# Kernel optimization log

Hardware: AMD Instinct MI355X
Metric: run time of the kernel (lower is better)

## Reference

```python
import jax, jax.numpy as jnp
import numpy as np

NUM_TOKENS = 8192
CODEBOOK_DIM = 64
ENC_CH = 512
DEC_CH = 512
B, H, W = 16, 32, 32


def setup_inputs() -> dict:
    key = jax.random.key(0)
    ks = jax.random.split(key, 6)
    return {
        "x": jax.random.normal(ks[0], (B, ENC_CH, H, W), dtype=jnp.float32),
        "w_in": jax.random.normal(ks[1], (CODEBOOK_DIM, ENC_CH), dtype=jnp.float32) * 0.05,
        "b_in": jax.random.normal(ks[2], (CODEBOOK_DIM,), dtype=jnp.float32) * 0.05,
        "embedding": jax.random.normal(ks[3], (NUM_TOKENS, CODEBOOK_DIM), dtype=jnp.float32),
        "w_out": jax.random.normal(ks[4], (DEC_CH, CODEBOOK_DIM), dtype=jnp.float32) * 0.05,
        "b_out": jax.random.normal(ks[5], (DEC_CH,), dtype=jnp.float32) * 0.05,
    }


def reference(x, w_in, b_in, embedding, w_out, b_out):
    # encoder projection: 1x1 conv == channel matmul. x: [B,C,H,W] -> [B,d,H,W]
    z = jnp.einsum('bchw,dc->bdhw', x, w_in) + b_in[None, :, None, None]

    # VectorQuantizer.forward -----------------------------------------
    # permute to channels-last and flatten: [B,H,W,d] -> [N,d]
    inputs = jnp.transpose(z, (0, 2, 3, 1))  # [B,H,W,d]
    flat = inputs.reshape(-1, CODEBOOK_DIM)  # [N,d]

    # squared L2 distances to every codebook entry: [N,K]
    distances = (jnp.sum(flat ** 2, axis=1, keepdims=True)
                 + jnp.sum(embedding ** 2, axis=1)[None, :]
                 - 2.0 * flat @ embedding.T)
    indices = jnp.argmin(distances, axis=1)  # [N] int

    # one-hot @ embedding in the original == direct gather
    quantized = jnp.take(embedding, indices, axis=0).reshape(inputs.shape)

    # straight-through estimator
    quantized = inputs + jax.lax.stop_gradient(quantized - inputs)
    tokens = jnp.transpose(quantized, (0, 3, 1, 2))  # [B,d,H,W]

    # decoder projection: 1x1 conv
    projected = jnp.einsum('bdhw,od->bohw', tokens, w_out) + b_out[None, :, None, None]
    return projected, indices
```

## Files before the change

kernel.cpp:

```cpp
#include <hip/hip_runtime.h>

#define NROWS 16384
#define DDIM 64
#define KCB 8192
#define CIN 512
#define OUTC 512
#define OUT_MAIN 8388608

typedef float f4 __attribute__((ext_vector_type(4)));
typedef float f32x16 __attribute__((ext_vector_type(16)));
typedef __bf16 bf16x4 __attribute__((ext_vector_type(4)));
typedef __bf16 bf16x8 __attribute__((ext_vector_type(8)));

#define OFF_ZBF 0
#define OFF_EBF 1572864
#define OFF_E2H 2359296
#define OFF_PMV 2367488
#define OFF_PMI 2629632
#define ZS_STRIDE 1048576
#define ES_STRIDE 524288

__global__ __launch_bounds__(256) void k_enc(const float* __restrict__ x,
                                             const float* __restrict__ w_in,
                                             const float* __restrict__ b_in,
                                             __bf16* __restrict__ zbf) {
  __shared__ float Wt[128][36];
  const int bid = blockIdx.x;
  const int g = bid >> 1, dh = bid & 1;
  const int b = g >> 5, h = g & 31;
  const int d0 = dh * 32;
  const int t = threadIdx.x;
  const int w = t & 31, dg = t >> 5;
  float acc[4];
#pragma unroll
  for (int j = 0; j < 4; ++j) acc[j] = b_in[d0 + dg * 4 + j];
  const float* xb = x + ((size_t)b * CIN * 1024) + h * 32 + w;
  for (int c0 = 0; c0 < CIN; c0 += 128) {
    __syncthreads();
#pragma unroll
    for (int i = 0; i < 16; ++i) {
      int e = t + 256 * i;
      int cc = e & 127, dd = e >> 7;
      Wt[cc][dd] = w_in[(size_t)(d0 + dd) * CIN + c0 + cc];
    }
    __syncthreads();
#pragma unroll 8
    for (int c = 0; c < 128; ++c) {
      float xv = xb[(size_t)(c0 + c) * 1024];
      const f4 wv = *(const f4*)&Wt[c][dg * 4];
      acc[0] = fmaf(xv, wv.x, acc[0]);
      acc[1] = fmaf(xv, wv.y, acc[1]);
      acc[2] = fmaf(xv, wv.z, acc[2]);
      acc[3] = fmaf(xv, wv.w, acc[3]);
    }
  }
  const int K0 = dh * 32 + dg * 4;
  const int kb = K0 >> 4, khalf = (K0 >> 3) & 1, j0 = K0 & 7;
  bf16x4 s0, s1, s2;
#pragma unroll
  for (int j = 0; j < 4; ++j) {
    float v = acc[j];
    __bf16 a0 = (__bf16)v;
    float r1 = v - (float)a0;
    __bf16 a1 = (__bf16)r1;
    float r2 = r1 - (float)a1;
    __bf16 a2 = (__bf16)r2;
    s0[j] = a0; s1[j] = a1; s2[j] = a2;
  }
  const size_t base = ((size_t)(kb * 512 + g) * 64 + khalf * 32 + w) * 8 + j0;
  *(bf16x4*)(zbf + base) = s0;
  *(bf16x4*)(zbf + base + ZS_STRIDE) = s1;
  *(bf16x4*)(zbf + base + 2 * ZS_STRIDE) = s2;
}

__global__ __launch_bounds__(256) void k_prep(const float* __restrict__ emb,
                                              __bf16* __restrict__ ebf,
                                              float* __restrict__ e2h) {
  __shared__ float s2[4][64];
  const int C0 = blockIdx.x * 64;
  const int t = threadIdx.x;
  const int cl = t & 63, kb = t >> 6;
  const int c = C0 + cl;
  const int cg = blockIdx.x * 2 + (cl >> 5);
  float e[16];
  {
    const f4* ep = (const f4*)(emb + (size_t)c * DDIM + kb * 16);
#pragma unroll
    for (int q = 0; q < 4; ++q) {
      f4 v = ep[q];
      e[q * 4 + 0] = v.x; e[q * 4 + 1] = v.y; e[q * 4 + 2] = v.z; e[q * 4 + 3] = v.w;
    }
  }
  float sq = 0.f;
#pragma unroll
  for (int i = 0; i < 16; ++i) sq = fmaf(e[i], e[i], sq);
  s2[kb][cl] = sq;
  bf16x8 v0[2], v1[2], v2[2];
#pragma unroll
  for (int i = 0; i < 16; ++i) {
    float v = e[i];
    __bf16 a0 = (__bf16)v;
    float r1 = v - (float)a0;
    __bf16 a1 = (__bf16)r1;
    float r2 = r1 - (float)a1;
    __bf16 a2 = (__bf16)r2;
    v0[i >> 3][i & 7] = a0; v1[i >> 3][i & 7] = a1; v2[i >> 3][i & 7] = a2;
  }
#pragma unroll
  for (int khalf = 0; khalf < 2; ++khalf) {
    const size_t dst = ((size_t)(kb * 256 + cg) * 64 + khalf * 32 + (cl & 31)) * 8;
    *(bf16x8*)(ebf + dst) = v0[khalf];
    *(bf16x8*)(ebf + dst + ES_STRIDE) = v1[khalf];
    *(bf16x8*)(ebf + dst + 2 * ES_STRIDE) = v2[khalf];
  }
  __syncthreads();
  if (t < 64)
    e2h[C0 + t] = 0.5f * (s2[0][t] + s2[1][t] + s2[2][t] + s2[3][t]);
}

__global__ __launch_bounds__(64, 2) void k_argmin(const __bf16* __restrict__ zbf,
                                                  const __bf16* __restrict__ ebf,
                                                  const float* __restrict__ e2h,
                                                  float* __restrict__ pmv,
                                                  int* __restrict__ pmi) {
  const int wid = blockIdx.x;
  const int rt = wid >> 4, chunk = wid & 15;
  const int R = rt * 64;
  const int l = threadIdx.x;
  const int h4 = (l >> 5) * 4;

  bf16x8 zf0[4][2], zf1[4][2], zf2[4][2];
#pragma unroll
  for (int kb = 0; kb < 4; ++kb)
#pragma unroll
    for (int rn = 0; rn < 2; ++rn) {
      const int g = (R >> 5) + rn;
      zf0[kb][rn] = *(const bf16x8*)(zbf + ((size_t)(kb * 512 + g) * 64 + l) * 8);
      zf1[kb][rn] = *(const bf16x8*)(zbf + ZS_STRIDE + ((size_t)(kb * 512 + g) * 64 + l) * 8);
      zf2[kb][rn] = *(const bf16x8*)(zbf + 2 * ZS_STRIDE + ((size_t)(kb * 512 + g) * 64 + l) * 8);
    }
  float mv0 = -3.4028235e38f, mv1 = -3.4028235e38f;
  int mi0 = 0, mi1 = 0;

#pragma unroll 1
  for (int st = 0; st < 8; ++st) {
    const int cbase = chunk * 512 + st * 64;
    const int cg0 = cbase >> 5;
    const float* e2p = e2h + cbase;
    f32x16 acc[2][2];
#pragma unroll
    for (int cm = 0; cm < 2; ++cm) {
#pragma unroll
      for (int q = 0; q < 4; ++q) {
        const f4 e2q = *(const f4*)(e2p + cm * 32 + h4 + q * 8);
#pragma unroll
        for (int i = 0; i < 4; ++i) {
          acc[cm][0][q * 4 + i] = -e2q[i];
          acc[cm][1][q * 4 + i] = -e2q[i];
        }
      }
    }

    bf16x8 af[4][2];
#define LOAD_AF(b)                                                                 \
  {                                                                                \
    _Pragma("unroll") for (int kb = 0; kb < 4; ++kb)                               \
        _Pragma("unroll") for (int cm = 0; cm < 2; ++cm) af[kb][cm] =              \
        *(const bf16x8*)(ebf + (size_t)(b)*ES_STRIDE +                             \
                         ((size_t)(kb * 256 + cg0 + cm) * 64 + l) * 8);            \
  }
#define SWEEP(ZF)                                                                  \
  {                                                                                \
    _Pragma("unroll") for (int kb = 0; kb < 4; ++kb)                               \
        _Pragma("unroll") for (int cm = 0; cm < 2; ++cm)                           \
        _Pragma("unroll") for (int rn = 0; rn < 2; ++rn) acc[cm][rn] =             \
        __builtin_amdgcn_mfma_f32_32x32x16_bf16(af[kb][cm], ZF[kb][rn],            \
                                                acc[cm][rn], 0, 0, 0);             \
  }
    LOAD_AF(0);
    SWEEP(zf0); SWEEP(zf1); SWEEP(zf2);
    LOAD_AF(1);
    SWEEP(zf0); SWEEP(zf1);
    LOAD_AF(2);
    SWEEP(zf0);
#undef LOAD_AF
#undef SWEEP
#pragma unroll
    for (int cm = 0; cm < 2; ++cm) {
#pragma unroll
      for (int q = 0; q < 4; ++q) {
#pragma unroll
        for (int i = 0; i < 4; ++i) {
          const int reg = q * 4 + i;
          const int code = cbase + cm * 32 + h4 + q * 8 + i;
          const float s0 = acc[cm][0][reg];
          if (s0 > mv0) { mv0 = s0; mi0 = code; }
          const float s1 = acc[cm][1][reg];
          if (s1 > mv1) { mv1 = s1; mi1 = code; }
        }
      }
    }
  }
  {
    float ov = __shfl_xor(mv0, 32); int oi = __shfl_xor(mi0, 32);
    if (ov > mv0 || (ov == mv0 && oi < mi0)) { mv0 = ov; mi0 = oi; }
    ov = __shfl_xor(mv1, 32); oi = __shfl_xor(mi1, 32);
    if (ov > mv1 || (ov == mv1 && oi < mi1)) { mv1 = ov; mi1 = oi; }
  }
  if (l < 32) {
    const int row0 = R + l, row1 = R + 32 + l;
    pmv[chunk * NROWS + row0] = mv0;
    pmi[chunk * NROWS + row0] = mi0;
    pmv[chunk * NROWS + row1] = mv1;
    pmi[chunk * NROWS + row1] = mi1;
  }
}

__global__ __launch_bounds__(256) void k_pick(const float* __restrict__ pmv,
                                              const int* __restrict__ pmi,
                                              float* __restrict__ idxf) {
  int n = blockIdx.x * 256 + threadIdx.x;
  float bv = pmv[n];
  int bi = pmi[n];
#pragma unroll
  for (int p = 1; p < 16; ++p) {
    float v = pmv[p * NROWS + n];
    int i = pmi[p * NROWS + n];
    if (v > bv) { bv = v; bi = i; }
  }
  idxf[n] = (float)bi;
}

__global__ __launch_bounds__(256) void k_dec(const float* __restrict__ emb,
                                             const float* __restrict__ w_out,
                                             const float* __restrict__ b_out,
                                             const float* __restrict__ idxf,
                                             float* __restrict__ out) {
  __shared__ float Qt[DDIM][36];
  __shared__ float Wt[DDIM][68];
  const int bid = blockIdx.x;
  const int bh = bid >> 1, oh = bid & 1;
  const int b = bh >> 5, h = bh & 31;
  const int t = threadIdx.x;
  const int w = t & 31, og = t >> 5;
  {
    const int dd = t & 63, r4 = t >> 6;
#pragma unroll
    for (int i = 0; i < 8; ++i) {
      int r = r4 + 4 * i;
      int qi = (int)idxf[bh * 32 + r];
      Qt[dd][r] = emb[(size_t)qi * DDIM + dd];
    }
  }
  for (int ob = 0; ob < 4; ++ob) {
    const int o0 = oh * 256 + ob * 64;
    __syncthreads();
#pragma unroll
    for (int i = 0; i < 16; ++i) {
      int e = t + 256 * i;
      int oo = e >> 6, dd = e & 63;
      Wt[dd][oo] = w_out[(size_t)(o0 + oo) * DDIM + dd];
    }
    __syncthreads();
    float a[8];
#pragma unroll
    for (int j = 0; j < 8; ++j) a[j] = b_out[o0 + og * 8 + j];
#pragma unroll 4
    for (int d = 0; d < 64; ++d) {
      float qv = Qt[d][w];
      const f4 w0 = *(const f4*)&Wt[d][og * 8];
      const f4 w1 = *(const f4*)&Wt[d][og * 8 + 4];
      a[0] = fmaf(qv, w0.x, a[0]);
      a[1] = fmaf(qv, w0.y, a[1]);
      a[2] = fmaf(qv, w0.z, a[2]);
      a[3] = fmaf(qv, w0.w, a[3]);
      a[4] = fmaf(qv, w1.x, a[4]);
      a[5] = fmaf(qv, w1.y, a[5]);
      a[6] = fmaf(qv, w1.z, a[6]);
      a[7] = fmaf(qv, w1.w, a[7]);
    }
    float* op = out + (((size_t)b * OUTC + o0 + og * 8) * 32 + h) * 32 + w;
#pragma unroll
    for (int j = 0; j < 8; ++j) op[(size_t)j * 1024] = a[j];
  }
}

extern "C" void kernel_launch(void* const* d_in, const int* in_sizes, int n_in,
                              void* d_out, int out_size, void* d_ws, size_t ws_size,
                              hipStream_t stream) {
  const float* x = (const float*)d_in[0];
  const float* w_in = (const float*)d_in[1];
  const float* b_in = (const float*)d_in[2];
  const float* emb = (const float*)d_in[3];
  const float* w_out = (const float*)d_in[4];
  const float* b_out = (const float*)d_in[5];
  float* out = (float*)d_out;

  __bf16* zbf = (__bf16*)(out + OFF_ZBF);
  __bf16* ebf = (__bf16*)(out + OFF_EBF);
  float* e2h = out + OFF_E2H;
  float* pmv = out + OFF_PMV;
  int* pmi = (int*)(out + OFF_PMI);
  float* idxf = out + OUT_MAIN;

  k_enc<<<1024, 256, 0, stream>>>(x, w_in, b_in, zbf);
  k_prep<<<128, 256, 0, stream>>>(emb, ebf, e2h);
  k_argmin<<<4096, 64, 0, stream>>>(zbf, ebf, e2h, pmv, pmi);
  k_pick<<<64, 256, 0, stream>>>(pmv, pmi, idxf);
  k_dec<<<1024, 256, 0, stream>>>(emb, w_out, b_out, idxf, out);
}
```

Measured before the change: 252.7 us.

## Share codebook tiles across four waves via double-buffered LDS in argmin

The argmin kernel moves from one 64-thread wave per block, each loading its own codebook fragments from global memory, to 256-thread blocks. The four waves (32 rows each) share a 32-code codebook tile that is staged into LDS with async global_load_lds and double-buffered across stages. This cuts redundant global and L2 codebook traffic and overlaps loads with MFMA work. In exchange each wave now holds a single 32x32 accumulator, so there is less MFMA work per fragment load, and every stage adds a block-wide barrier.

Result: faster. 242.6 us (-4.0%).

```diff
diff --git a/kernel.cpp b/kernel.cpp
--- a/kernel.cpp
+++ b/kernel.cpp
@@ -118,101 +118,91 @@
     e2h[C0 + t] = 0.5f * (s2[0][t] + s2[1][t] + s2[2][t] + s2[3][t]);
 }
 
-__global__ __launch_bounds__(64, 2) void k_argmin(const __bf16* __restrict__ zbf,
-                                                  const __bf16* __restrict__ ebf,
-                                                  const float* __restrict__ e2h,
-                                                  float* __restrict__ pmv,
-                                                  int* __restrict__ pmi) {
-  const int wid = blockIdx.x;
-  const int rt = wid >> 4, chunk = wid & 15;
-  const int R = rt * 64;
-  const int l = threadIdx.x;
+__global__ __launch_bounds__(256, 3) void k_argmin(const __bf16* __restrict__ zbf,
+                                                   const __bf16* __restrict__ ebf,
+                                                   const float* __restrict__ e2h,
+                                                   float* __restrict__ pmv,
+                                                   int* __restrict__ pmi) {
+  __shared__ __bf16 Als[2][6144];
+  const int bid = blockIdx.x;
+  const int rowblk = bid >> 4, chunk = bid & 15;
+  const int t = threadIdx.x;
+  const int l = t & 63;
+  const int wv = t >> 6;
   const int h4 = (l >> 5) * 4;
-
-  bf16x8 zf0[4][2], zf1[4][2], zf2[4][2];
-#pragma unroll
-  for (int kb = 0; kb < 4; ++kb)
-#pragma unroll
-    for (int rn = 0; rn < 2; ++rn) {
-      const int g = (R >> 5) + rn;
-      zf0[kb][rn] = *(const bf16x8*)(zbf + ((size_t)(kb * 512 + g) * 64 + l) * 8);
-      zf1[kb][rn] = *(const bf16x8*)(zbf + ZS_STRIDE + ((size_t)(kb * 512 + g) * 64 + l) * 8);
-      zf2[kb][rn] = *(const bf16x8*)(zbf + 2 * ZS_STRIDE + ((size_t)(kb * 512 + g) * 64 + l) * 8);
-    }
-  float mv0 = -3.4028235e38f, mv1 = -3.4028235e38f;
-  int mi0 = 0, mi1 = 0;
-
+  const int g = rowblk * 4 + wv;
+
+  bf16x8 zf[3][4];
+#pragma unroll
+  for (int s = 0; s < 3; ++s)
+#pragma unroll
+    for (int kb = 0; kb < 4; ++kb)
+      zf[s][kb] = *(const bf16x8*)(zbf + (size_t)s * ZS_STRIDE +
+                                   ((size_t)(kb * 512 + g) * 64 + l) * 8);
+
+  float mv = -3.4028235e38f;
+  int mi = 0;
+
+  auto stage = [&](int st, int bi) {
+    const int cg = chunk * 16 + st;
+#pragma unroll
+    for (int i = 0; i < 3; ++i) {
+      const int fi = wv * 3 + i;
+      const int s = fi >> 2, kb = fi & 3;
+      const __bf16* src = ebf + (size_t)s * ES_STRIDE +
+                          ((size_t)(kb * 256 + cg) * 64 + l) * 8;
+      __builtin_amdgcn_global_load_lds(
+          (const __attribute__((address_space(1))) void*)src,
+          (__attribute__((address_space(3))) void*)&Als[bi][fi * 512 + l * 8],
+          16, 0, 0);
+    }
+  };
+
+  stage(0, 0);
 #pragma unroll 1
-  for (int st = 0; st < 8; ++st) {
-    const int cbase = chunk * 512 + st * 64;
-    const int cg0 = cbase >> 5;
-    const float* e2p = e2h + cbase;
-    f32x16 acc[2][2];
-#pragma unroll
-    for (int cm = 0; cm < 2; ++cm) {
-#pragma unroll
-      for (int q = 0; q < 4; ++q) {
-        const f4 e2q = *(const f4*)(e2p + cm * 32 + h4 + q * 8);
-#pragma unroll
-        for (int i = 0; i < 4; ++i) {
-          acc[cm][0][q * 4 + i] = -e2q[i];
-          acc[cm][1][q * 4 + i] = -e2q[i];
-        }
+  for (int st = 0; st < 16; ++st) {
+    __syncthreads();
+    if (st + 1 < 16) stage(st + 1, (st + 1) & 1);
+    const __bf16* B = &Als[st & 1][0];
+    const int cbase = (chunk * 16 + st) * 32;
+    f32x16 acc = (f32x16)(0.0f);
+    bf16x8 af[4];
+#define LDAF(b)                                                              \
+  {                                                                          \
+    _Pragma("unroll") for (int kb = 0; kb < 4; ++kb) af[kb] =                \
+        *(const bf16x8*)(B + ((b)*4 + kb) * 512 + l * 8);                    \
+  }
+#define SW(a)                                                                \
+  {                                                                          \
+    _Pragma("unroll") for (int kb = 0; kb < 4; ++kb) acc =                   \
+        __builtin_amdgcn_mfma_f32_32x32x16_bf16(af[kb], zf[a][kb], acc, 0,   \
+                                                0, 0);                       \
+  }
+    LDAF(0); SW(0); SW(1); SW(2);
+    LDAF(1); SW(0); SW(1);
+    LDAF(2); SW(0);
+#undef LDAF
+#undef SW
+    const float* e2p = e2h + cbase + h4;
+#pragma unroll
+    for (int q = 0; q < 4; ++q) {
+      const f4 e2q = *(const f4*)(e2p + q * 8);
+#pragma unroll
+      for (int i = 0; i < 4; ++i) {
+        const float s = acc[q * 4 + i] - e2q[i];
+        if (s > mv) { mv = s; mi = cbase + h4 + q * 8 + i; }
       }
     }
-
-    bf16x8 af[4][2];
-#define LOAD_AF(b)                                                                 \
-  {                                                                                \
-    _Pragma("unroll") for (int kb = 0; kb < 4; ++kb)                               \
-        _Pragma("unroll") for (int cm = 0; cm < 2; ++cm) af[kb][cm] =              \
-        *(const bf16x8*)(ebf + (size_t)(b)*ES_STRIDE +                             \
-                         ((size_t)(kb * 256 + cg0 + cm) * 64 + l) * 8);            \
-  }
-#define SWEEP(ZF)                                                                  \
-  {                                                                                \
-    _Pragma("unroll") for (int kb = 0; kb < 4; ++kb)                               \
-        _Pragma("unroll") for (int cm = 0; cm < 2; ++cm)                           \
-        _Pragma("unroll") for (int rn = 0; rn < 2; ++rn) acc[cm][rn] =             \
-        __builtin_amdgcn_mfma_f32_32x32x16_bf16(af[kb][cm], ZF[kb][rn],            \
-                                                acc[cm][rn], 0, 0, 0);             \
-  }
-    LOAD_AF(0);
-    SWEEP(zf0); SWEEP(zf1); SWEEP(zf2);
-    LOAD_AF(1);
-    SWEEP(zf0); SWEEP(zf1);
-    LOAD_AF(2);
-    SWEEP(zf0);
-#undef LOAD_AF
-#undef SWEEP
-#pragma unroll
-    for (int cm = 0; cm < 2; ++cm) {
-#pragma unroll
-      for (int q = 0; q < 4; ++q) {
-#pragma unroll
-        for (int i = 0; i < 4; ++i) {
-          const int reg = q * 4 + i;
-          const int code = cbase + cm * 32 + h4 + q * 8 + i;
-          const float s0 = acc[cm][0][reg];
-          if (s0 > mv0) { mv0 = s0; mi0 = code; }
-          const float s1 = acc[cm][1][reg];
-          if (s1 > mv1) { mv1 = s1; mi1 = code; }
-        }
-      }
-    }
   }
   {
-    float ov = __shfl_xor(mv0, 32); int oi = __shfl_xor(mi0, 32);
-    if (ov > mv0 || (ov == mv0 && oi < mi0)) { mv0 = ov; mi0 = oi; }
-    ov = __shfl_xor(mv1, 32); oi = __shfl_xor(mi1, 32);
-    if (ov > mv1 || (ov == mv1 && oi < mi1)) { mv1 = ov; mi1 = oi; }
+    float ov = __shfl_xor(mv, 32);
+    int oi = __shfl_xor(mi, 32);
+    if (ov > mv || (ov == mv && oi < mi)) { mv = ov; mi = oi; }
   }
   if (l < 32) {
-    const int row0 = R + l, row1 = R + 32 + l;
-    pmv[chunk * NROWS + row0] = mv0;
-    pmi[chunk * NROWS + row0] = mi0;
-    pmv[chunk * NROWS + row1] = mv1;
-    pmi[chunk * NROWS + row1] = mi1;
+    const int row = rowblk * 128 + wv * 32 + l;
+    pmv[chunk * NROWS + row] = mv;
+    pmi[chunk * NROWS + row] = mi;
   }
 }
 
@@ -305,7 +295,7 @@
 
   k_enc<<<1024, 256, 0, stream>>>(x, w_in, b_in, zbf);
   k_prep<<<128, 256, 0, stream>>>(emb, ebf, e2h);
-  k_argmin<<<4096, 64, 0, stream>>>(zbf, ebf, e2h, pmv, pmi);
+  k_argmin<<<2048, 256, 0, stream>>>(zbf, ebf, e2h, pmv, pmi);
   k_pick<<<64, 256, 0, stream>>>(pmv, pmi, idxf);
   k_dec<<<1024, 256, 0, stream>>>(emb, w_out, b_out, idxf, out);
 }
```
